# Optimization experiments

Measured on AMD Instinct MI355X. Metric: run time of the kernel, lower is better.

Reference implementation:

```python
import jax, jax.numpy as jnp
import numpy as np


def _gcn_conv(x, W, b, src, dst, num_nodes):
    # PyG GCNConv: linear transform, add self-loops, symmetric normalization,
    # scatter-sum aggregation, then bias.
    h = x @ W  # [N, out]
    loop = jnp.arange(num_nodes, dtype=src.dtype)
    s = jnp.concatenate([src, loop])
    d = jnp.concatenate([dst, loop])
    deg = jax.ops.segment_sum(jnp.ones_like(s, dtype=h.dtype), d, num_segments=num_nodes)
    dinv = jnp.where(deg > 0, jax.lax.rsqrt(deg), 0.0)
    norm = dinv[s] * dinv[d]  # [E+N]
    msgs = h[s] * norm[:, None]  # gather + scale
    out = jax.ops.segment_sum(msgs, d, num_segments=num_nodes)
    return out + b


def setup_inputs() -> dict:
    key = jax.random.key(0)
    k1, k2, k3, k4 = jax.random.split(key, 4)
    N, F_in, H, C, E = 100000, 512, 16, 40, 3200000
    node_feature = jax.random.normal(k1, (N, F_in), dtype=jnp.float32)
    W1 = jax.random.normal(k2, (F_in, H), dtype=jnp.float32) * (1.0 / np.sqrt(F_in))
    b1 = jnp.zeros((H,), dtype=jnp.float32)
    W2 = jax.random.normal(k3, (H, C), dtype=jnp.float32) * (1.0 / np.sqrt(H))
    b2 = jnp.zeros((C,), dtype=jnp.float32)
    edge_index = jax.random.randint(k4, (2, E), 0, N, dtype=jnp.int64)
    return {"node_feature": node_feature, "W1": W1, "b1": b1,
            "W2": W2, "b2": b2, "edge_index": edge_index}


def reference(node_feature, W1, b1, W2, b2, edge_index):
    # Inference path: F.dropout(training=False) is identity.
    N = node_feature.shape[0]
    src, dst = edge_index[0], edge_index[1]
    x = jax.nn.elu(_gcn_conv(node_feature, W1, b1, src, dst, N))
    x = _gcn_conv(x, W2, b2, src, dst, N)
    return jax.nn.log_softmax(x, axis=1)
```

## Files before the change

kernel.cpp:

```cpp
#include <hip/hip_runtime.h>
#include <hip/hip_bf16.h>
#include <math.h>

__device__ __forceinline__ unsigned pk_bf16(float lo, float hi) {
    unsigned a = __float_as_uint(lo), b = __float_as_uint(hi);
    unsigned alo = (a + 0x7fffu + ((a >> 16) & 1u)) >> 16;
    unsigned bhi = (b + 0x7fffu + ((b >> 16) & 1u)) >> 16;
    return alo | (bhi << 16);
}
__device__ __forceinline__ float bf_lo(unsigned u) { return __uint_as_float(u << 16); }
__device__ __forceinline__ float bf_hi(unsigned u) { return __uint_as_float(u & 0xffff0000u); }


__global__ __launch_bounds__(256) void k_count(const int* __restrict__ dst,
                                               int* __restrict__ countsT,
                                               int E, int B, int NBLK, int CHUNK) {
    __shared__ int hist[1024];
    int tid = threadIdx.x, b = blockIdx.x;
    for (int j = tid; j < B; j += 256) hist[j] = 0;
    __syncthreads();
    int e0 = b * CHUNK, e1 = min(e0 + CHUNK, E);
    for (int i = e0 + tid * 4; i < e1; i += 1024) {
        if (i + 3 < e1) {
            int4 d4 = *(const int4*)(dst + i);
            atomicAdd(&hist[d4.x >> 7], 1);
            atomicAdd(&hist[d4.y >> 7], 1);
            atomicAdd(&hist[d4.z >> 7], 1);
            atomicAdd(&hist[d4.w >> 7], 1);
        } else {
            for (int k = i; k < e1; ++k) atomicAdd(&hist[dst[k] >> 7], 1);
        }
    }
    __syncthreads();
    for (int j = tid; j < B; j += 256) countsT[j * NBLK + b] = hist[j];
}

__global__ __launch_bounds__(256) void k_scanb(int* __restrict__ countsT,
                                               int* __restrict__ btotal, int NBLK) {
    __shared__ int sm[256];
    int j = blockIdx.x, tid = threadIdx.x;
    int v = (tid < NBLK) ? countsT[j * NBLK + tid] : 0;
    sm[tid] = v; __syncthreads();
    for (int off = 1; off < 256; off <<= 1) {
        int t = (tid >= off) ? sm[tid - off] : 0;
        __syncthreads(); sm[tid] += t; __syncthreads();
    }
    if (tid < NBLK) countsT[j * NBLK + tid] = sm[tid] - v;
    if (tid == 255) btotal[j] = sm[255];
}

__global__ __launch_bounds__(1024) void k_scanb2(const int* __restrict__ btotal,
                                                 int* __restrict__ bstart,
                                                 int* __restrict__ offs,
                                                 int B, int E, int N) {
    __shared__ int sm[1024];
    int tid = threadIdx.x;
    int v = (tid < B) ? btotal[tid] : 0;
    sm[tid] = v; __syncthreads();
    for (int off = 1; off < 1024; off <<= 1) {
        int t = (tid >= off) ? sm[tid - off] : 0;
        __syncthreads(); sm[tid] += t; __syncthreads();
    }
    if (tid < B) bstart[tid] = sm[tid] - v;
    if (tid == 0) { bstart[B] = E; offs[N] = E; }
}

__global__ __launch_bounds__(256) void k_place(const int* __restrict__ src,
                                               const int* __restrict__ dst,
                                               const int* __restrict__ countsT,
                                               const int* __restrict__ bstart,
                                               unsigned* __restrict__ ebuf,
                                               int E, int B, int NBLK, int CHUNK) {
    __shared__ int cur[1024];
    int tid = threadIdx.x, b = blockIdx.x;
    for (int j = tid; j < B; j += 256) cur[j] = bstart[j] + countsT[j * NBLK + b];
    __syncthreads();
    int e0 = b * CHUNK, e1 = min(e0 + CHUNK, E);
    for (int i = e0 + tid * 4; i < e1; i += 1024) {
        if (i + 3 < e1) {
            int4 d4 = *(const int4*)(dst + i);
            int4 s4 = *(const int4*)(src + i);
            int p0 = atomicAdd(&cur[d4.x >> 7], 1);
            int p1 = atomicAdd(&cur[d4.y >> 7], 1);
            int p2 = atomicAdd(&cur[d4.z >> 7], 1);
            int p3 = atomicAdd(&cur[d4.w >> 7], 1);
            ebuf[p0] = ((unsigned)(d4.x & 127) << 17) | (unsigned)s4.x;
            ebuf[p1] = ((unsigned)(d4.y & 127) << 17) | (unsigned)s4.y;
            ebuf[p2] = ((unsigned)(d4.z & 127) << 17) | (unsigned)s4.z;
            ebuf[p3] = ((unsigned)(d4.w & 127) << 17) | (unsigned)s4.w;
        } else {
            for (int k = i; k < e1; ++k) {
                int d = dst[k], s = src[k];
                int pos = atomicAdd(&cur[d >> 7], 1);
                ebuf[pos] = ((unsigned)(d & 127) << 17) | (unsigned)s;
            }
        }
    }
}

__global__ __launch_bounds__(256) void k_csr(const int* __restrict__ bstart,
                                             const unsigned* __restrict__ ebuf,
                                             int* __restrict__ csr,
                                             int* __restrict__ offs,
                                             float* __restrict__ dinv, int N) {
    __shared__ int sm[128];
    __shared__ int loc[128];
    int j = blockIdx.x, tid = threadIdx.x;
    int e0 = bstart[j], e1 = bstart[j + 1];
    if (tid < 128) sm[tid] = 0;
    __syncthreads();
    for (int i = e0 + tid; i < e1; i += 256) atomicAdd(&sm[ebuf[i] >> 17], 1);
    __syncthreads();
    int v = (tid < 128) ? sm[tid] : 0;
    for (int off = 1; off < 128; off <<= 1) {
        int t = (tid < 128 && tid >= off) ? sm[tid - off] : 0;
        __syncthreads();
        if (tid < 128) sm[tid] += t;
        __syncthreads();
    }
    if (tid < 128) {
        int ex = sm[tid] - v;
        loc[tid] = e0 + ex;
        int n = j * 128 + tid;
        if (n < N) {
            offs[n] = e0 + ex;
            dinv[n] = rsqrtf((float)v + 1.0f);
        }
    }
    __syncthreads();
    for (int i = e0 + tid; i < e1; i += 256) {
        unsigned eb = ebuf[i];
        int pos = atomicAdd(&loc[eb >> 17], 1);
        csr[pos] = (int)(eb & 0x1FFFFu);
    }
}

__global__ __launch_bounds__(256) void k_gemm1(
    const float* __restrict__ x, const float* __restrict__ W1,
    const float* __restrict__ dinv, unsigned* __restrict__ h1s, int N)
{
    __shared__ float4 lds4[4][128];
    const int lane = threadIdx.x & 63;
    const int wid  = threadIdx.x >> 6;
    const int g = lane >> 4, j = lane & 15;
    const int gwave  = blockIdx.x * 4 + wid;
    const int nwaves = gridDim.x * 4;

    float w[128];
    #pragma unroll
    for (int t = 0; t < 128; ++t) w[t] = W1[(g * 128 + t) * 16 + j];

    float* buf = (float*)lds4[wid];
    int row = gwave;
    if (row >= N) return;
    const float4* xr = (const float4*)(x + (size_t)row * 512);
    float4 a = xr[lane], b = xr[lane + 64];
    while (row < N) {
        int nrow = row + nwaves;
        float4 a2, b2;
        if (nrow < N) {
            const float4* xr2 = (const float4*)(x + (size_t)nrow * 512);
            a2 = xr2[lane]; b2 = xr2[lane + 64];
        }
        ((float4*)buf)[lane]      = a;
        ((float4*)buf)[lane + 64] = b;
        asm volatile("s_waitcnt lgkmcnt(0)" ::: "memory");
        const float4* bx = (const float4*)(buf + g * 128);
        float acc = 0.f;
        #pragma unroll
        for (int s = 0; s < 32; ++s) {
            float4 xv = bx[s];
            acc = fmaf(xv.x, w[4*s+0], acc);
            acc = fmaf(xv.y, w[4*s+1], acc);
            acc = fmaf(xv.z, w[4*s+2], acc);
            acc = fmaf(xv.w, w[4*s+3], acc);
        }
        acc += __shfl_xor(acc, 16);
        acc += __shfl_xor(acc, 32);
        float hv = 0.f;
        if (lane < 16) hv = acc * dinv[row];
        float oth = __shfl_xor(hv, 1);
        if (lane < 16 && !(lane & 1))
            h1s[(size_t)row * 8 + (j >> 1)] = pk_bf16(hv, oth);
        asm volatile("s_waitcnt lgkmcnt(0)" ::: "memory");
        row = nrow;
        a = a2; b = b2;
    }
}

__global__ __launch_bounds__(256) void k_l1(
    const int* __restrict__ offs, const int* __restrict__ csr,
    const unsigned* __restrict__ h1s, const float* __restrict__ dinv,
    const float* __restrict__ b1, unsigned* __restrict__ x1s, int N)
{
    const int lane = threadIdx.x & 63;
    const int wid  = threadIdx.x >> 6;
    const int gwave  = blockIdx.x * 4 + wid;
    const int nwaves = gridDim.x * 4;
    const int eg = lane >> 3, w = lane & 7;
    const float b1v = b1[lane & 15];

    for (int n = gwave; n < N; n += nwaves) {
        int o0 = offs[n], cnt = offs[n + 1] - o0;
        float accx = 0.f, accy = 0.f;
        for (int cb = 0; cb < cnt; cb += 64) {
            int cs = cnt - cb; if (cs > 64) cs = 64;
            int sreg = (lane < cs) ? csr[o0 + cb + lane] : 0;
            #pragma unroll
            for (int i = 0; i < 8; ++i) {
                int e = i * 8 + eg;
                int s = __shfl(sreg, e);
                if (e < cs) {
                    unsigned u = h1s[(size_t)s * 8 + w];
                    accx += bf_lo(u);
                    accy += bf_hi(u);
                }
            }
        }
        accx += __shfl_xor(accx, 8);  accy += __shfl_xor(accy, 8);
        accx += __shfl_xor(accx, 16); accy += __shfl_xor(accy, 16);
        accx += __shfl_xor(accx, 32); accy += __shfl_xor(accy, 32);

        float dv = dinv[n];
        float fx = __shfl(accx, lane >> 1), fy = __shfl(accy, lane >> 1);
        float xv = 0.f;
        if (lane < 16) {
            float aggv = (lane & 1) ? fy : fx;
            unsigned su = h1s[(size_t)n * 8 + (lane >> 1)];
            float self = (lane & 1) ? bf_hi(su) : bf_lo(su);
            xv = (aggv + self) * dv + b1v;
            xv = xv > 0.f ? xv : expm1f(xv);
            xv *= dv;
        }
        float oth = __shfl_xor(xv, 1);
        if (lane < 16 && !(lane & 1))
            x1s[(size_t)n * 8 + (lane >> 1)] = pk_bf16(xv, oth);
    }
}

__global__ __launch_bounds__(256) void k_l2(
    const int* __restrict__ offs, const int* __restrict__ csr,
    const unsigned* __restrict__ x1s, const float* __restrict__ dinv,
    const float* __restrict__ W2, const float* __restrict__ b2,
    float* __restrict__ out, int N)
{
    const int lane = threadIdx.x & 63;
    const int wid  = threadIdx.x >> 6;
    const int gwave  = blockIdx.x * 4 + wid;
    const int nwaves = gridDim.x * 4;
    const int eg = lane >> 3, w = lane & 7;
    const int c = lane < 40 ? lane : 39;

    float w2[16];
    #pragma unroll
    for (int t = 0; t < 16; ++t) w2[t] = W2[t * 40 + c];
    const float b2v = b2[c];

    for (int n = gwave; n < N; n += nwaves) {
        int o0 = offs[n], cnt = offs[n + 1] - o0;
        float accx = 0.f, accy = 0.f;
        for (int cb = 0; cb < cnt; cb += 64) {
            int cs = cnt - cb; if (cs > 64) cs = 64;
            int sreg = (lane < cs) ? csr[o0 + cb + lane] : 0;
            #pragma unroll
            for (int i = 0; i < 8; ++i) {
                int e = i * 8 + eg;
                int s = __shfl(sreg, e);
                if (e < cs) {
                    unsigned u = x1s[(size_t)s * 8 + w];
                    accx += bf_lo(u);
                    accy += bf_hi(u);
                }
            }
        }
        accx += __shfl_xor(accx, 8);  accy += __shfl_xor(accy, 8);
        accx += __shfl_xor(accx, 16); accy += __shfl_xor(accy, 16);
        accx += __shfl_xor(accx, 32); accy += __shfl_xor(accy, 32);

        float dv = dinv[n];
        float fx = __shfl(accx, lane >> 1), fy = __shfl(accy, lane >> 1);
        float xv = 0.f;
        if (lane < 16) {
            float aggv = (lane & 1) ? fy : fx;
            unsigned su = x1s[(size_t)n * 8 + (lane >> 1)];
            float self = (lane & 1) ? bf_hi(su) : bf_lo(su);
            xv = (aggv + self) * dv;
        }
        float v = b2v;
        #pragma unroll
        for (int t = 0; t < 16; ++t)
            v = fmaf(__shfl(xv, t), w2[t], v);

        float vm = (lane < 40) ? v : -INFINITY;
        #pragma unroll
        for (int off = 32; off; off >>= 1) vm = fmaxf(vm, __shfl_xor(vm, off));
        float ex = (lane < 40) ? expf(v - vm) : 0.f;
        float sum = ex;
        #pragma unroll
        for (int off = 32; off; off >>= 1) sum += __shfl_xor(sum, off);
        if (lane < 40) out[(size_t)n * 40 + lane] = v - vm - logf(sum);
    }
}

extern "C" void kernel_launch(void* const* d_in, const int* in_sizes, int n_in,
                              void* d_out, int out_size, void* d_ws, size_t ws_size,
                              hipStream_t stream) {
    const float* x  = (const float*)d_in[0];
    const float* W1 = (const float*)d_in[1];
    const float* b1 = (const float*)d_in[2];
    const float* W2 = (const float*)d_in[3];
    const float* b2 = (const float*)d_in[4];
    const int*   ei = (const int*)d_in[5];

    const int N = in_sizes[0] / 512;
    const int E = in_sizes[5] / 2;
    const int* src = ei;
    const int* dst = ei + E;

    const int B     = (N + 127) >> 7;
    const int CHUNK = 16384;
    const int NBLK  = (E + CHUNK - 1) / CHUNK;

    int*      countsT = (int*)d_ws;
    int*      btotal  = countsT + (size_t)B * NBLK;
    int*      bstart  = btotal + B;
    unsigned* ebuf    = (unsigned*)(bstart + B + 4);
    int*      csr     = (int*)(ebuf + E);
    int*      offs    = csr + E;
    float*    dinv    = (float*)(offs + N + 4);
    unsigned* h1s     = (unsigned*)(dinv + N);
    unsigned* x1s     = h1s + (size_t)8 * N;
    float*    out     = (float*)d_out;

    k_count <<<NBLK, 256, 0, stream>>>(dst, countsT, E, B, NBLK, CHUNK);
    k_scanb <<<B, 256, 0, stream>>>(countsT, btotal, NBLK);
    k_scanb2<<<1, 1024, 0, stream>>>(btotal, bstart, offs, B, E, N);
    k_place <<<NBLK, 256, 0, stream>>>(src, dst, countsT, bstart, ebuf, E, B, NBLK, CHUNK);
    k_csr   <<<B, 256, 0, stream>>>(bstart, ebuf, csr, offs, dinv, N);
    k_gemm1 <<<2048, 256, 0, stream>>>(x, W1, dinv, h1s, N);
    k_l1    <<<2048, 256, 0, stream>>>(offs, csr, h1s, dinv, b1, x1s, N);
    k_l2    <<<2048, 256, 0, stream>>>(offs, csr, x1s, dinv, W2, b2, out, N);
}
```

Baseline: 268.8 us.

## Stage GEMM rows via async global-to-LDS loads, widen gathers to 16-byte

The first-layer GEMM now loads 8-row tiles into a double-buffered LDS region with global_load_lds, so the next tile's load overlaps the current tile's compute. It replaces per-wave register prefetch with block-wide synchronisation. Both aggregation kernels now gather each neighbour's 16-feature bf16 row as two 16-byte loads per lane pair instead of eight 4-byte loads, which means more accumulators and a longer shuffle reduction. The histogram chunk size is halved, doubling the block count, and the per-bucket scan widens to 512 threads to handle the larger count.

```diff
diff --git a/kernel.cpp b/kernel.cpp
--- a/kernel.cpp
+++ b/kernel.cpp
@@ -10,6 +10,12 @@
 }
 __device__ __forceinline__ float bf_lo(unsigned u) { return __uint_as_float(u << 16); }
 __device__ __forceinline__ float bf_hi(unsigned u) { return __uint_as_float(u & 0xffff0000u); }
+
+__device__ __forceinline__ void gload16(const void* gsrc, void* ldst) {
+    __builtin_amdgcn_global_load_lds(
+        (const __attribute__((address_space(1))) unsigned*)gsrc,
+        (__attribute__((address_space(3))) unsigned*)ldst, 16, 0, 0);
+}
 
 
 __global__ __launch_bounds__(256) void k_count(const int* __restrict__ dst,
@@ -35,18 +41,18 @@
     for (int j = tid; j < B; j += 256) countsT[j * NBLK + b] = hist[j];
 }
 
-__global__ __launch_bounds__(256) void k_scanb(int* __restrict__ countsT,
+__global__ __launch_bounds__(512) void k_scanb(int* __restrict__ countsT,
                                                int* __restrict__ btotal, int NBLK) {
-    __shared__ int sm[256];
+    __shared__ int sm[512];
     int j = blockIdx.x, tid = threadIdx.x;
     int v = (tid < NBLK) ? countsT[j * NBLK + tid] : 0;
     sm[tid] = v; __syncthreads();
-    for (int off = 1; off < 256; off <<= 1) {
+    for (int off = 1; off < 512; off <<= 1) {
         int t = (tid >= off) ? sm[tid - off] : 0;
         __syncthreads(); sm[tid] += t; __syncthreads();
     }
     if (tid < NBLK) countsT[j * NBLK + tid] = sm[tid] - v;
-    if (tid == 255) btotal[j] = sm[255];
+    if (tid == 511) btotal[j] = sm[511];
 }
 
 __global__ __launch_bounds__(1024) void k_scanb2(const int* __restrict__ btotal,
@@ -139,52 +145,66 @@
     const float* __restrict__ x, const float* __restrict__ W1,
     const float* __restrict__ dinv, unsigned* __restrict__ h1s, int N)
 {
-    __shared__ float4 lds4[4][128];
-    const int lane = threadIdx.x & 63;
-    const int wid  = threadIdx.x >> 6;
+    __shared__ float buf[2][8 * 512];
+    const int tid  = threadIdx.x;
+    const int lane = tid & 63;
+    const int wid  = tid >> 6;
     const int g = lane >> 4, j = lane & 15;
-    const int gwave  = blockIdx.x * 4 + wid;
-    const int nwaves = gridDim.x * 4;
 
     float w[128];
     #pragma unroll
     for (int t = 0; t < 128; ++t) w[t] = W1[(g * 128 + t) * 16 + j];
 
-    float* buf = (float*)lds4[wid];
-    int row = gwave;
-    if (row >= N) return;
-    const float4* xr = (const float4*)(x + (size_t)row * 512);
-    float4 a = xr[lane], b = xr[lane + 64];
-    while (row < N) {
-        int nrow = row + nwaves;
-        float4 a2, b2;
-        if (nrow < N) {
-            const float4* xr2 = (const float4*)(x + (size_t)nrow * 512);
-            a2 = xr2[lane]; b2 = xr2[lane + 64];
-        }
-        ((float4*)buf)[lane]      = a;
-        ((float4*)buf)[lane + 64] = b;
-        asm volatile("s_waitcnt lgkmcnt(0)" ::: "memory");
-        const float4* bx = (const float4*)(buf + g * 128);
-        float acc = 0.f;
-        #pragma unroll
-        for (int s = 0; s < 32; ++s) {
-            float4 xv = bx[s];
-            acc = fmaf(xv.x, w[4*s+0], acc);
-            acc = fmaf(xv.y, w[4*s+1], acc);
-            acc = fmaf(xv.z, w[4*s+2], acc);
-            acc = fmaf(xv.w, w[4*s+3], acc);
-        }
-        acc += __shfl_xor(acc, 16);
-        acc += __shfl_xor(acc, 32);
-        float hv = 0.f;
-        if (lane < 16) hv = acc * dinv[row];
-        float oth = __shfl_xor(hv, 1);
-        if (lane < 16 && !(lane & 1))
-            h1s[(size_t)row * 8 + (j >> 1)] = pk_bf16(hv, oth);
-        asm volatile("s_waitcnt lgkmcnt(0)" ::: "memory");
-        row = nrow;
-        a = a2; b = b2;
+    const int TT = (N + 7) >> 3;
+
+    auto stage = [&](int t, int b) {
+        int r0 = t * 8;
+        if (r0 + 8 <= N) {
+            char* lbase = (char*)&buf[b][0] + wid * 4096;
+            const char* gbase = (const char*)(x + (size_t)r0 * 512) + wid * 4096 + lane * 16;
+            #pragma unroll
+            for (int i = 0; i < 4; ++i)
+                gload16(gbase + i * 1024, lbase + i * 1024);
+        } else {
+            int nv = (N - r0) * 512;
+            for (int idx = tid * 4; idx < nv; idx += 1024)
+                *(float4*)&buf[b][idx] = *(const float4*)(x + (size_t)r0 * 512 + idx);
+        }
+    };
+
+    int t = blockIdx.x;
+    if (t >= TT) return;
+    stage(t, 0);
+    __syncthreads();
+    int cur = 0;
+    for (; t < TT; t += gridDim.x) {
+        int tn = t + gridDim.x;
+        if (tn < TT) stage(tn, cur ^ 1);
+        #pragma unroll
+        for (int rr = 0; rr < 2; ++rr) {
+            int row = t * 8 + wid * 2 + rr;
+            if (row < N) {
+                const float4* bx = (const float4*)(&buf[cur][(wid * 2 + rr) * 512 + g * 128]);
+                float acc = 0.f;
+                #pragma unroll
+                for (int s = 0; s < 32; ++s) {
+                    float4 xv = bx[s];
+                    acc = fmaf(xv.x, w[4*s+0], acc);
+                    acc = fmaf(xv.y, w[4*s+1], acc);
+                    acc = fmaf(xv.z, w[4*s+2], acc);
+                    acc = fmaf(xv.w, w[4*s+3], acc);
+                }
+                acc += __shfl_xor(acc, 16);
+                acc += __shfl_xor(acc, 32);
+                float hv = 0.f;
+                if (lane < 16) hv = acc * dinv[row];
+                float oth = __shfl_xor(hv, 1);
+                if (lane < 16 && !(lane & 1))
+                    h1s[(size_t)row * 8 + (j >> 1)] = pk_bf16(hv, oth);
+            }
+        }
+        __syncthreads();
+        cur ^= 1;
     }
 }
 
@@ -197,44 +217,54 @@
     const int wid  = threadIdx.x >> 6;
     const int gwave  = blockIdx.x * 4 + wid;
     const int nwaves = gridDim.x * 4;
-    const int eg = lane >> 3, w = lane & 7;
-    const float b1v = b1[lane & 15];
+    const int e2 = lane >> 1, w = lane & 1;
+    const uint4* h14 = (const uint4*)h1s;
+
+    float b1r[8];
+    #pragma unroll
+    for (int k = 0; k < 8; ++k) b1r[k] = b1[w * 8 + k];
 
     for (int n = gwave; n < N; n += nwaves) {
         int o0 = offs[n], cnt = offs[n + 1] - o0;
-        float accx = 0.f, accy = 0.f;
+        float acc[8] = {0.f,0.f,0.f,0.f,0.f,0.f,0.f,0.f};
         for (int cb = 0; cb < cnt; cb += 64) {
             int cs = cnt - cb; if (cs > 64) cs = 64;
             int sreg = (lane < cs) ? csr[o0 + cb + lane] : 0;
             #pragma unroll
-            for (int i = 0; i < 8; ++i) {
-                int e = i * 8 + eg;
+            for (int i = 0; i < 2; ++i) {
+                int e = i * 32 + e2;
                 int s = __shfl(sreg, e);
                 if (e < cs) {
-                    unsigned u = h1s[(size_t)s * 8 + w];
-                    accx += bf_lo(u);
-                    accy += bf_hi(u);
+                    uint4 u = h14[(size_t)s * 2 + w];
+                    acc[0] += bf_lo(u.x); acc[1] += bf_hi(u.x);
+                    acc[2] += bf_lo(u.y); acc[3] += bf_hi(u.y);
+                    acc[4] += bf_lo(u.z); acc[5] += bf_hi(u.z);
+                    acc[6] += bf_lo(u.w); acc[7] += bf_hi(u.w);
                 }
             }
         }
-        accx += __shfl_xor(accx, 8);  accy += __shfl_xor(accy, 8);
-        accx += __shfl_xor(accx, 16); accy += __shfl_xor(accy, 16);
-        accx += __shfl_xor(accx, 32); accy += __shfl_xor(accy, 32);
-
-        float dv = dinv[n];
-        float fx = __shfl(accx, lane >> 1), fy = __shfl(accy, lane >> 1);
-        float xv = 0.f;
-        if (lane < 16) {
-            float aggv = (lane & 1) ? fy : fx;
-            unsigned su = h1s[(size_t)n * 8 + (lane >> 1)];
-            float self = (lane & 1) ? bf_hi(su) : bf_lo(su);
-            xv = (aggv + self) * dv + b1v;
-            xv = xv > 0.f ? xv : expm1f(xv);
-            xv *= dv;
-        }
-        float oth = __shfl_xor(xv, 1);
-        if (lane < 16 && !(lane & 1))
-            x1s[(size_t)n * 8 + (lane >> 1)] = pk_bf16(xv, oth);
+        #pragma unroll
+        for (int st = 2; st <= 32; st <<= 1) {
+            #pragma unroll
+            for (int k = 0; k < 8; ++k) acc[k] += __shfl_xor(acc[k], st);
+        }
+        if (lane < 2) {
+            float dv = dinv[n];
+            uint4 su = h14[(size_t)n * 2 + lane];
+            float sf[8] = {bf_lo(su.x),bf_hi(su.x),bf_lo(su.y),bf_hi(su.y),
+                           bf_lo(su.z),bf_hi(su.z),bf_lo(su.w),bf_hi(su.w)};
+            uint4 pk;
+            unsigned* pw = (unsigned*)&pk;
+            #pragma unroll
+            for (int k2 = 0; k2 < 4; ++k2) {
+                float v0 = (acc[2*k2]   + sf[2*k2])   * dv + b1r[2*k2];
+                v0 = v0 > 0.f ? v0 : expm1f(v0);  v0 *= dv;
+                float v1 = (acc[2*k2+1] + sf[2*k2+1]) * dv + b1r[2*k2+1];
+                v1 = v1 > 0.f ? v1 : expm1f(v1);  v1 *= dv;
+                pw[k2] = pk_bf16(v0, v1);
+            }
+            ((uint4*)x1s)[(size_t)n * 2 + lane] = pk;
+        }
     }
 }
 
@@ -248,8 +278,9 @@
     const int wid  = threadIdx.x >> 6;
     const int gwave  = blockIdx.x * 4 + wid;
     const int nwaves = gridDim.x * 4;
-    const int eg = lane >> 3, w = lane & 7;
+    const int e2 = lane >> 1, w = lane & 1;
     const int c = lane < 40 ? lane : 39;
+    const uint4* x14 = (const uint4*)x1s;
 
     float w2[16];
     #pragma unroll
@@ -258,38 +289,39 @@
 
     for (int n = gwave; n < N; n += nwaves) {
         int o0 = offs[n], cnt = offs[n + 1] - o0;
-        float accx = 0.f, accy = 0.f;
+        float acc[8] = {0.f,0.f,0.f,0.f,0.f,0.f,0.f,0.f};
         for (int cb = 0; cb < cnt; cb += 64) {
             int cs = cnt - cb; if (cs > 64) cs = 64;
             int sreg = (lane < cs) ? csr[o0 + cb + lane] : 0;
             #pragma unroll
-            for (int i = 0; i < 8; ++i) {
-                int e = i * 8 + eg;
+            for (int i = 0; i < 2; ++i) {
+                int e = i * 32 + e2;
                 int s = __shfl(sreg, e);
                 if (e < cs) {
-                    unsigned u = x1s[(size_t)s * 8 + w];
-                    accx += bf_lo(u);
-                    accy += bf_hi(u);
+                    uint4 u = x14[(size_t)s * 2 + w];
+                    acc[0] += bf_lo(u.x); acc[1] += bf_hi(u.x);
+                    acc[2] += bf_lo(u.y); acc[3] += bf_hi(u.y);
+                    acc[4] += bf_lo(u.z); acc[5] += bf_hi(u.z);
+                    acc[6] += bf_lo(u.w); acc[7] += bf_hi(u.w);
                 }
             }
         }
-        accx += __shfl_xor(accx, 8);  accy += __shfl_xor(accy, 8);
-        accx += __shfl_xor(accx, 16); accy += __shfl_xor(accy, 16);
-        accx += __shfl_xor(accx, 32); accy += __shfl_xor(accy, 32);
-
+        #pragma unroll
+        for (int st = 2; st <= 32; st <<= 1) {
+            #pragma unroll
+            for (int k = 0; k < 8; ++k) acc[k] += __shfl_xor(acc[k], st);
+        }
         float dv = dinv[n];
-        float fx = __shfl(accx, lane >> 1), fy = __shfl(accy, lane >> 1);
-        float xv = 0.f;
-        if (lane < 16) {
-            float aggv = (lane & 1) ? fy : fx;
-            unsigned su = x1s[(size_t)n * 8 + (lane >> 1)];
-            float self = (lane & 1) ? bf_hi(su) : bf_lo(su);
-            xv = (aggv + self) * dv;
-        }
+        uint4 su = x14[(size_t)n * 2 + w];
+        float s8[8] = {bf_lo(su.x),bf_hi(su.x),bf_lo(su.y),bf_hi(su.y),
+                       bf_lo(su.z),bf_hi(su.z),bf_lo(su.w),bf_hi(su.w)};
+        #pragma unroll
+        for (int k = 0; k < 8; ++k) s8[k] = (acc[k] + s8[k]) * dv;
+
         float v = b2v;
         #pragma unroll
         for (int t = 0; t < 16; ++t)
-            v = fmaf(__shfl(xv, t), w2[t], v);
+            v = fmaf(__shfl(s8[t & 7], t >> 3), w2[t], v);
 
         float vm = (lane < 40) ? v : -INFINITY;
         #pragma unroll
@@ -318,7 +350,7 @@
     const int* dst = ei + E;
 
     const int B     = (N + 127) >> 7;
-    const int CHUNK = 16384;
+    const int CHUNK = 8192;
     const int NBLK  = (E + CHUNK - 1) / CHUNK;
 
     int*      countsT = (int*)d_ws;
@@ -333,11 +365,11 @@
     float*    out     = (float*)d_out;
 
     k_count <<<NBLK, 256, 0, stream>>>(dst, countsT, E, B, NBLK, CHUNK);
-    k_scanb <<<B, 256, 0, stream>>>(countsT, btotal, NBLK);
+    k_scanb <<<B, 512, 0, stream>>>(countsT, btotal, NBLK);
     k_scanb2<<<1, 1024, 0, stream>>>(btotal, bstart, offs, B, E, N);
     k_place <<<NBLK, 256, 0, stream>>>(src, dst, countsT, bstart, ebuf, E, B, NBLK, CHUNK);
     k_csr   <<<B, 256, 0, stream>>>(bstart, ebuf, csr, offs, dinv, N);
-    k_gemm1 <<<2048, 256, 0, stream>>>(x, W1, dinv, h1s, N);
+    k_gemm1 <<<1024, 256, 0, stream>>>(x, W1, dinv, h1s, N);
     k_l1    <<<2048, 256, 0, stream>>>(offs, csr, h1s, dinv, b1, x1s, N);
     k_l2    <<<2048, 256, 0, stream>>>(offs, csr, x1s, dinv, W2, b2, out, N);
 }
```

Measured after the change: 318.2 us. 1.18x slower.
